# Kernel optimization log

Hardware: AMD Instinct MI355X
Metric: run time of the kernel (lower is better)

Reference implementation:

```python
import jax, jax.numpy as jnp
import numpy as np

N = 50000   # nodes
E = 800000  # edges (avg degree 16)
D = 128     # node_dim == hidden_dim
L = 5       # propagation_depth


def setup_inputs() -> dict:
    key = jax.random.key(0)
    k1, k2, k3, k4 = jax.random.split(key, 4)
    feat = jax.random.normal(k1, (N, D), dtype=jnp.float32)
    src = jax.random.randint(k2, (E,), 0, N)
    dst = jax.random.randint(k3, (E,), 0, N)
    # Glorot-ish init for the 5 stacked GraphConv weights
    W = jax.random.normal(k4, (L, D, D), dtype=jnp.float32) * (1.0 / np.sqrt(D))
    b = jnp.zeros((L, D), dtype=jnp.float32)
    return {"feat": feat, "src": src, "dst": dst, "W": W, "b": b}


def reference(feat, src, dst, W, b):
    # DGL GraphConv, norm='both':
    #   h' = relu( D_in^{-1/2} * (sum over in-edges of D_out^{-1/2} h_src) @ W + b )
    ones = jnp.ones((src.shape[0],), dtype=feat.dtype)
    deg_out = jnp.maximum(jax.ops.segment_sum(ones, src, num_segments=N), 1.0)
    deg_in = jnp.maximum(jax.ops.segment_sum(ones, dst, num_segments=N), 1.0)
    norm_src = deg_out ** -0.5  # [N]
    norm_dst = deg_in ** -0.5   # [N]

    h = feat
    for l in range(W.shape[0]):
        hs = h * norm_src[:, None]                                   # [N, D]
        agg = jax.ops.segment_sum(hs[src], dst, num_segments=N)      # sparse SpMM: [N, D]
        h = jax.nn.relu(agg * norm_dst[:, None] @ W[l] + b[l])       # [N, D]
    return h
```

## Files before the change

kernel.cpp:

```cpp
#include <hip/hip_runtime.h>

#define DD 128
#define NBC 64

__device__ __forceinline__ unsigned int rtn16(float f) {
  unsigned int u = __float_as_uint(f);
  return (u + 0x7FFFu + ((u >> 16) & 1u)) >> 16;
}
#define UNPK_LO(u) __uint_as_float((u) << 16)
#define UNPK_HI(u) __uint_as_float((u) & 0xFFFF0000u)


__global__ __launch_bounds__(256) void hist2_kernel(const int* __restrict__ src,
                                                    const int* __restrict__ dst,
                                                    unsigned int* __restrict__ hsrc,
                                                    unsigned int* __restrict__ hdst,
                                                    int e, int n, int ec) {
  __shared__ unsigned int h[32768];
  int c = blockIdx.x & (NBC - 1);
  bool is_src = blockIdx.x >= NBC;
  const int* __restrict__ ids = is_src ? src : dst;
  unsigned int* __restrict__ out = is_src ? hsrc : hdst;
  int nw = (n + 1) >> 1;
  for (int w = threadIdx.x; w < nw; w += 256) h[w] = 0u;
  __syncthreads();
  int lo = c * ec;
  int hi = lo + ec; if (hi > e) hi = e;
  for (int i = lo + threadIdx.x; i < hi; i += 256) {
    int d = ids[i];
    atomicAdd(&h[d >> 1], (d & 1) ? 0x10000u : 1u);
  }
  __syncthreads();
  for (int w = threadIdx.x; w < nw; w += 256) out[(size_t)c * nw + w] = h[w];
}

__global__ __launch_bounds__(256) void degnorm_prefix_kernel(
    const unsigned int* __restrict__ hsrc, unsigned int* __restrict__ hdst,
    int* __restrict__ deg_in, float* __restrict__ norm_src,
    float* __restrict__ norm_dst, int n) {
  int nw = (n + 1) >> 1;
  int w = blockIdx.x * 256 + threadIdx.x;
  if (w >= nw) return;
  unsigned int slo = 0, shi = 0, dlo = 0, dhi = 0;
  for (int c = 0; c < NBC; ++c) {
    unsigned int a = hsrc[(size_t)c * nw + w];
    slo += a & 0xFFFFu; shi += a >> 16;
    size_t idx = (size_t)c * nw + w;
    unsigned int v = hdst[idx];
    hdst[idx] = dlo | (dhi << 16);
    dlo += v & 0xFFFFu; dhi += v >> 16;
  }
  int n0 = 2 * w, n1 = 2 * w + 1;
  deg_in[n0] = (int)dlo;
  norm_src[n0] = 1.0f / sqrtf((float)(slo < 1u ? 1u : slo));
  norm_dst[n0] = 1.0f / sqrtf((float)(dlo < 1u ? 1u : dlo));
  if (n1 < n) {
    deg_in[n1] = (int)dhi;
    norm_src[n1] = 1.0f / sqrtf((float)(shi < 1u ? 1u : shi));
    norm_dst[n1] = 1.0f / sqrtf((float)(dhi < 1u ? 1u : dhi));
  }
}

__global__ __launch_bounds__(256) void scan_partial_kernel(const int* __restrict__ cnt,
                                                           int* __restrict__ bsum, int n) {
  __shared__ int ws[4];
  int tid = threadIdx.x;
  int base = blockIdx.x * 2048 + tid * 8;
  int s = 0;
#pragma unroll
  for (int i = 0; i < 8; ++i) {
    int id = base + i;
    if (id < n) s += cnt[id];
  }
#pragma unroll
  for (int d = 32; d; d >>= 1) s += __shfl_xor(s, d, 64);
  int lane = tid & 63, wid = tid >> 6;
  if (lane == 0) ws[wid] = s;
  __syncthreads();
  if (tid == 0) bsum[blockIdx.x] = ws[0] + ws[1] + ws[2] + ws[3];
}

__global__ __launch_bounds__(64) void scan_bsum_kernel(int* __restrict__ bsum, int nb) {
  int lane = threadIdx.x;
  int run = 0;
  for (int base = 0; base < nb; base += 64) {
    int id = base + lane;
    int v = (id < nb) ? bsum[id] : 0;
    int sc = v;
#pragma unroll
    for (int d = 1; d < 64; d <<= 1) {
      int t = __shfl_up(sc, d, 64);
      if (lane >= d) sc += t;
    }
    if (id < nb) bsum[id] = run + sc - v;
    run += __shfl(sc, 63, 64);
  }
}

__global__ __launch_bounds__(256) void scan_final_kernel(const int* __restrict__ cnt,
                                                         const int* __restrict__ bsum,
                                                         int* __restrict__ row_ptr,
                                                         int n, int e_total) {
  __shared__ int ws[4];
  int tid = threadIdx.x, lane = tid & 63, wid = tid >> 6;
  int base = blockIdx.x * 2048 + tid * 8;
  int v[8];
  int s = 0;
#pragma unroll
  for (int i = 0; i < 8; ++i) {
    int id = base + i;
    v[i] = (id < n) ? cnt[id] : 0;
    s += v[i];
  }
  int sc = s;
#pragma unroll
  for (int d = 1; d < 64; d <<= 1) {
    int t = __shfl_up(sc, d, 64);
    if (lane >= d) sc += t;
  }
  if (lane == 63) ws[wid] = sc;
  __syncthreads();
  int woff = 0;
  for (int w = 0; w < wid; ++w) woff += ws[w];
  int off = bsum[blockIdx.x] + woff + (sc - s);
#pragma unroll
  for (int i = 0; i < 8; ++i) {
    int id = base + i;
    if (id < n) {
      row_ptr[id] = off;
      off += v[i];
    }
  }
  if (blockIdx.x == 0 && tid == 0) row_ptr[n] = e_total;
}

__global__ __launch_bounds__(256) void fillx_kernel(const int* __restrict__ src,
                                                    const int* __restrict__ dst,
                                                    const unsigned int* __restrict__ hdst,
                                                    const int* __restrict__ row_ptr,
                                                    int* __restrict__ adj,
                                                    int e, int n, int ec) {
  __shared__ unsigned int h[32768];
  int c = blockIdx.x;
  int nw = (n + 1) >> 1;
  for (int w = threadIdx.x; w < nw; w += 256) h[w] = 0u;
  __syncthreads();
  int lo = c * ec;
  int hi = lo + ec; if (hi > e) hi = e;
  for (int i = lo + threadIdx.x; i < hi; i += 256) {
    int s = src[i];
    int d = dst[i];
    unsigned int old = atomicAdd(&h[d >> 1], (d & 1) ? 0x10000u : 1u);
    unsigned int rank = (d & 1) ? (old >> 16) : (old & 0xFFFFu);
    unsigned int pre = hdst[(size_t)c * nw + (d >> 1)];
    pre = (d & 1) ? (pre >> 16) : (pre & 0xFFFFu);
    adj[row_ptr[d] + (int)pre + (int)rank] = s;
  }
}

__global__ __launch_bounds__(256) void prescale_kernel(const float* __restrict__ feat,
                                                       const float* __restrict__ ns,
                                                       unsigned short* __restrict__ ga,
                                                       unsigned short* __restrict__ gb,
                                                       int n) {
  int i = blockIdx.x * 256 + threadIdx.x;
  if (i >= (n + 1) * 32) return;
  if (i >= n * 32) {
    ((uint2*)ga)[i] = make_uint2(0u, 0u);
    ((uint2*)gb)[i] = make_uint2(0u, 0u);
    return;
  }
  float4 v = ((const float4*)feat)[i];
  float s = ns[i >> 5];
  unsigned int p0 = rtn16(v.x * s), p1 = rtn16(v.y * s);
  unsigned int p2 = rtn16(v.z * s), p3 = rtn16(v.w * s);
  ((uint2*)ga)[i] = make_uint2(p0 | (p1 << 16), p2 | (p3 << 16));
}

__global__ __launch_bounds__(256) void layer_kernel(const unsigned short* __restrict__ gin,
                                                    unsigned short* __restrict__ goutb,
                                                    float* __restrict__ goutf,
                                                    const int* __restrict__ adj,
                                                    const int* __restrict__ row_ptr,
                                                    const float* __restrict__ ns,
                                                    const float* __restrict__ ndv,
                                                    const float* __restrict__ W,
                                                    const float* __restrict__ bias,
                                                    int n, int last) {
  __shared__ float Xs[32][DD];
  int tid = threadIdx.x;
  int lane = tid & 63;
  int wv = tid >> 6;
  int m4 = lane & 15;
  int q = lane >> 4;
  int row0 = blockIdx.x * 32;
  const uint4* g4 = (const uint4*)gin;

  for (int r = wv; r < 32; r += 4) {
    int node = row0 + r;
    float a0 = 0.f, a1 = 0.f, a2 = 0.f, a3 = 0.f;
    float a4 = 0.f, a5 = 0.f, a6 = 0.f, a7 = 0.f;
    float scale = 0.f;
#define ACC8(v)                                        \
  a0 += UNPK_LO(v.x); a1 += UNPK_HI(v.x);              \
  a2 += UNPK_LO(v.y); a3 += UNPK_HI(v.y);              \
  a4 += UNPK_LO(v.z); a5 += UNPK_HI(v.z);              \
  a6 += UNPK_LO(v.w); a7 += UNPK_HI(v.w);
    if (node < n) {
      scale = ndv[node];
      int beg = row_ptr[node];
      int end = row_ptr[node + 1];
      for (int j = beg; j < end; j += 16) {
        int i0 = j + q;
        int i1 = j + 4 + q;
        int i2 = j + 8 + q;
        int i3 = j + 12 + q;
        int e0 = (i0 < end) ? adj[i0] : n;
        int e1 = (i1 < end) ? adj[i1] : n;
        int e2 = (i2 < end) ? adj[i2] : n;
        int e3 = (i3 < end) ? adj[i3] : n;
        uint4 v0 = g4[(size_t)e0 * 16 + m4];
        uint4 v1 = g4[(size_t)e1 * 16 + m4];
        uint4 v2 = g4[(size_t)e2 * 16 + m4];
        uint4 v3 = g4[(size_t)e3 * 16 + m4];
        ACC8(v0); ACC8(v1); ACC8(v2); ACC8(v3);
      }
    }
#undef ACC8
    a0 += __shfl_xor(a0, 16, 64); a0 += __shfl_xor(a0, 32, 64);
    a1 += __shfl_xor(a1, 16, 64); a1 += __shfl_xor(a1, 32, 64);
    a2 += __shfl_xor(a2, 16, 64); a2 += __shfl_xor(a2, 32, 64);
    a3 += __shfl_xor(a3, 16, 64); a3 += __shfl_xor(a3, 32, 64);
    a4 += __shfl_xor(a4, 16, 64); a4 += __shfl_xor(a4, 32, 64);
    a5 += __shfl_xor(a5, 16, 64); a5 += __shfl_xor(a5, 32, 64);
    a6 += __shfl_xor(a6, 16, 64); a6 += __shfl_xor(a6, 32, 64);
    a7 += __shfl_xor(a7, 16, 64); a7 += __shfl_xor(a7, 32, 64);
    if (q == 0) {
      float* xp = &Xs[r][m4 * 8];
      xp[0] = a0 * scale; xp[1] = a1 * scale;
      xp[2] = a2 * scale; xp[3] = a3 * scale;
      xp[4] = a4 * scale; xp[5] = a5 * scale;
      xp[6] = a6 * scale; xp[7] = a7 * scale;
    }
  }
  __syncthreads();

  int tx = tid & 31;
  int ty = tid >> 5;
  float acc[4][4] = {};
  const float4* wp0 = (const float4*)W + tx;
  for (int k4 = 0; k4 < DD / 4; ++k4) {
    const float4* wp = wp0 + (size_t)k4 * 4 * 32;
    float4 w0 = wp[0];
    float4 w1 = wp[32];
    float4 w2 = wp[64];
    float4 w3 = wp[96];
#pragma unroll
    for (int i = 0; i < 4; ++i) {
      float4 x = *(const float4*)&Xs[ty * 4 + i][k4 * 4];
      acc[i][0] = fmaf(x.x, w0.x, acc[i][0]);
      acc[i][1] = fmaf(x.x, w0.y, acc[i][1]);
      acc[i][2] = fmaf(x.x, w0.z, acc[i][2]);
      acc[i][3] = fmaf(x.x, w0.w, acc[i][3]);
      acc[i][0] = fmaf(x.y, w1.x, acc[i][0]);
      acc[i][1] = fmaf(x.y, w1.y, acc[i][1]);
      acc[i][2] = fmaf(x.y, w1.z, acc[i][2]);
      acc[i][3] = fmaf(x.y, w1.w, acc[i][3]);
      acc[i][0] = fmaf(x.z, w2.x, acc[i][0]);
      acc[i][1] = fmaf(x.z, w2.y, acc[i][1]);
      acc[i][2] = fmaf(x.z, w2.z, acc[i][2]);
      acc[i][3] = fmaf(x.z, w2.w, acc[i][3]);
      acc[i][0] = fmaf(x.w, w3.x, acc[i][0]);
      acc[i][1] = fmaf(x.w, w3.y, acc[i][1]);
      acc[i][2] = fmaf(x.w, w3.z, acc[i][2]);
      acc[i][3] = fmaf(x.w, w3.w, acc[i][3]);
    }
  }
  float4 bv = *(const float4*)(bias + tx * 4);
#pragma unroll
  for (int i = 0; i < 4; ++i) {
    int r = row0 + ty * 4 + i;
    if (r < n) {
      float4 o;
      o.x = fmaxf(acc[i][0] + bv.x, 0.f);
      o.y = fmaxf(acc[i][1] + bv.y, 0.f);
      o.z = fmaxf(acc[i][2] + bv.z, 0.f);
      o.w = fmaxf(acc[i][3] + bv.w, 0.f);
      if (last) {
        *(float4*)(goutf + (size_t)r * DD + tx * 4) = o;
      } else {
        float s = ns[r];
        unsigned int p0 = rtn16(o.x * s), p1 = rtn16(o.y * s);
        unsigned int p2 = rtn16(o.z * s), p3 = rtn16(o.w * s);
        ((uint2*)(goutb + (size_t)r * DD))[tx] =
            make_uint2(p0 | (p1 << 16), p2 | (p3 << 16));
      }
    }
  }
}


extern "C" void kernel_launch(void* const* d_in, const int* in_sizes, int n_in,
                              void* d_out, int out_size, void* d_ws, size_t ws_size,
                              hipStream_t stream) {
  const float* feat = (const float*)d_in[0];
  const int* src = (const int*)d_in[1];
  const int* dst = (const int*)d_in[2];
  const float* W = (const float*)d_in[3];
  const float* b = (const float*)d_in[4];
  const int N = in_sizes[0] / DD;
  const int E = in_sizes[1];
  const int L = in_sizes[3] / (DD * DD);
  const int NW = (N + 1) >> 1;
  const int EC = (E + NBC - 1) / NBC;

  char* p = (char*)d_ws;
  auto alloc = [&](size_t bytes) {
    void* r = (void*)p;
    p += (bytes + 255) & ~(size_t)255;
    return r;
  };
  int* deg_in = (int*)alloc((size_t)N * 4);
  int* row_ptr = (int*)alloc(((size_t)N + 1) * 4);
  int* adj = (int*)alloc((size_t)E * 4);
  float* norm_src = (float*)alloc((size_t)N * 4);
  float* norm_dst = (float*)alloc((size_t)N * 4);
  int* bsum = (int*)alloc(((size_t)N / 2048 + 2) * 4);
  unsigned int* hsrc = (unsigned int*)alloc((size_t)NBC * NW * 4);
  unsigned int* hdst = (unsigned int*)alloc((size_t)NBC * NW * 4);
  unsigned short* ga = (unsigned short*)alloc(((size_t)N + 1) * DD * 2);
  unsigned short* gb = (unsigned short*)alloc(((size_t)N + 1) * DD * 2);

  const int nb = (N + 2047) / 2048;
  const int nwb = (NW + 255) / 256;

  hist2_kernel<<<2 * NBC, 256, 0, stream>>>(src, dst, hsrc, hdst, E, N, EC);
  degnorm_prefix_kernel<<<nwb, 256, 0, stream>>>(hsrc, hdst, deg_in, norm_src,
                                                 norm_dst, N);
  scan_partial_kernel<<<nb, 256, 0, stream>>>(deg_in, bsum, N);
  scan_bsum_kernel<<<1, 64, 0, stream>>>(bsum, nb);
  scan_final_kernel<<<nb, 256, 0, stream>>>(deg_in, bsum, row_ptr, N, E);
  fillx_kernel<<<NBC, 256, 0, stream>>>(src, dst, hdst, row_ptr, adj, E, N, EC);

  float* out_f = (float*)d_out;
  prescale_kernel<<<((N + 1) * 32 + 255) / 256, 256, 0, stream>>>(feat, norm_src,
                                                                  ga, gb, N);
  for (int l = 0; l < L; ++l) {
    const unsigned short* gi = (l & 1) ? gb : ga;
    unsigned short* go = (l & 1) ? ga : gb;
    int last = (l == L - 1) ? 1 : 0;
    layer_kernel<<<(N + 31) / 32, 256, 0, stream>>>(
        gi, go, out_f, adj, row_ptr, norm_src, norm_dst,
        W + (size_t)l * DD * DD, b + (size_t)l * DD, N, last);
  }
}
```

Baseline: 435.2 us.

## Fuse scan partials into degree kernel and batch two-row neighbor gathers

The per-block degree sums for the row-pointer scan are now computed inside the degree/normalization kernel, which removes the separate scan_partial pass. The scan blocks shrink to 512 nodes so they line up with that kernel's blocks. The layer kernel's gather loop now handles two rows per wave at once and issues the first 32 neighbor index loads and feature loads for each row up front, to raise memory-level parallelism. It also sets a 4-blocks-per-SM launch bound. This costs higher register pressure and may cause spilling.

```diff
diff --git a/kernel.cpp b/kernel.cpp
--- a/kernel.cpp
+++ b/kernel.cpp
@@ -37,44 +37,36 @@
 __global__ __launch_bounds__(256) void degnorm_prefix_kernel(
     const unsigned int* __restrict__ hsrc, unsigned int* __restrict__ hdst,
     int* __restrict__ deg_in, float* __restrict__ norm_src,
-    float* __restrict__ norm_dst, int n) {
+    float* __restrict__ norm_dst, int* __restrict__ bsum, int n) {
+  __shared__ int ws[4];
   int nw = (n + 1) >> 1;
-  int w = blockIdx.x * 256 + threadIdx.x;
-  if (w >= nw) return;
+  int tid = threadIdx.x, lane = tid & 63, wid = tid >> 6;
+  int w = blockIdx.x * 256 + tid;
   unsigned int slo = 0, shi = 0, dlo = 0, dhi = 0;
-  for (int c = 0; c < NBC; ++c) {
-    unsigned int a = hsrc[(size_t)c * nw + w];
-    slo += a & 0xFFFFu; shi += a >> 16;
-    size_t idx = (size_t)c * nw + w;
-    unsigned int v = hdst[idx];
-    hdst[idx] = dlo | (dhi << 16);
-    dlo += v & 0xFFFFu; dhi += v >> 16;
-  }
-  int n0 = 2 * w, n1 = 2 * w + 1;
-  deg_in[n0] = (int)dlo;
-  norm_src[n0] = 1.0f / sqrtf((float)(slo < 1u ? 1u : slo));
-  norm_dst[n0] = 1.0f / sqrtf((float)(dlo < 1u ? 1u : dlo));
-  if (n1 < n) {
-    deg_in[n1] = (int)dhi;
-    norm_src[n1] = 1.0f / sqrtf((float)(shi < 1u ? 1u : shi));
-    norm_dst[n1] = 1.0f / sqrtf((float)(dhi < 1u ? 1u : dhi));
-  }
-}
-
-__global__ __launch_bounds__(256) void scan_partial_kernel(const int* __restrict__ cnt,
-                                                           int* __restrict__ bsum, int n) {
-  __shared__ int ws[4];
-  int tid = threadIdx.x;
-  int base = blockIdx.x * 2048 + tid * 8;
-  int s = 0;
-#pragma unroll
-  for (int i = 0; i < 8; ++i) {
-    int id = base + i;
-    if (id < n) s += cnt[id];
-  }
+  if (w < nw) {
+    for (int c = 0; c < NBC; ++c) {
+      unsigned int a = hsrc[(size_t)c * nw + w];
+      slo += a & 0xFFFFu; shi += a >> 16;
+      size_t idx = (size_t)c * nw + w;
+      unsigned int v = hdst[idx];
+      hdst[idx] = dlo | (dhi << 16);
+      dlo += v & 0xFFFFu; dhi += v >> 16;
+    }
+    int n0 = 2 * w, n1 = 2 * w + 1;
+    deg_in[n0] = (int)dlo;
+    norm_src[n0] = 1.0f / sqrtf((float)(slo < 1u ? 1u : slo));
+    norm_dst[n0] = 1.0f / sqrtf((float)(dlo < 1u ? 1u : dlo));
+    if (n1 < n) {
+      deg_in[n1] = (int)dhi;
+      norm_src[n1] = 1.0f / sqrtf((float)(shi < 1u ? 1u : shi));
+      norm_dst[n1] = 1.0f / sqrtf((float)(dhi < 1u ? 1u : dhi));
+    } else {
+      dhi = 0;
+    }
+  }
+  int s = (int)(dlo + dhi);
 #pragma unroll
   for (int d = 32; d; d >>= 1) s += __shfl_xor(s, d, 64);
-  int lane = tid & 63, wid = tid >> 6;
   if (lane == 0) ws[wid] = s;
   __syncthreads();
   if (tid == 0) bsum[blockIdx.x] = ws[0] + ws[1] + ws[2] + ws[3];
@@ -103,15 +95,10 @@
                                                          int n, int e_total) {
   __shared__ int ws[4];
   int tid = threadIdx.x, lane = tid & 63, wid = tid >> 6;
-  int base = blockIdx.x * 2048 + tid * 8;
-  int v[8];
-  int s = 0;
-#pragma unroll
-  for (int i = 0; i < 8; ++i) {
-    int id = base + i;
-    v[i] = (id < n) ? cnt[id] : 0;
-    s += v[i];
-  }
+  int id0 = blockIdx.x * 512 + tid * 2;
+  int v0 = (id0 < n) ? cnt[id0] : 0;
+  int v1 = (id0 + 1 < n) ? cnt[id0 + 1] : 0;
+  int s = v0 + v1;
   int sc = s;
 #pragma unroll
   for (int d = 1; d < 64; d <<= 1) {
@@ -121,16 +108,10 @@
   if (lane == 63) ws[wid] = sc;
   __syncthreads();
   int woff = 0;
-  for (int w = 0; w < wid; ++w) woff += ws[w];
+  for (int w2 = 0; w2 < wid; ++w2) woff += ws[w2];
   int off = bsum[blockIdx.x] + woff + (sc - s);
-#pragma unroll
-  for (int i = 0; i < 8; ++i) {
-    int id = base + i;
-    if (id < n) {
-      row_ptr[id] = off;
-      off += v[i];
-    }
-  }
+  if (id0 < n) row_ptr[id0] = off;
+  if (id0 + 1 < n) row_ptr[id0 + 1] = off + v0;
   if (blockIdx.x == 0 && tid == 0) row_ptr[n] = e_total;
 }
 
@@ -177,16 +158,12 @@
   ((uint2*)ga)[i] = make_uint2(p0 | (p1 << 16), p2 | (p3 << 16));
 }
 
-__global__ __launch_bounds__(256) void layer_kernel(const unsigned short* __restrict__ gin,
-                                                    unsigned short* __restrict__ goutb,
-                                                    float* __restrict__ goutf,
-                                                    const int* __restrict__ adj,
-                                                    const int* __restrict__ row_ptr,
-                                                    const float* __restrict__ ns,
-                                                    const float* __restrict__ ndv,
-                                                    const float* __restrict__ W,
-                                                    const float* __restrict__ bias,
-                                                    int n, int last) {
+__global__ __launch_bounds__(256, 4) void layer_kernel(
+    const unsigned short* __restrict__ gin, unsigned short* __restrict__ goutb,
+    float* __restrict__ goutf, const int* __restrict__ adj,
+    const int* __restrict__ row_ptr, const float* __restrict__ ns,
+    const float* __restrict__ ndv, const float* __restrict__ W,
+    const float* __restrict__ bias, int n, int last) {
   __shared__ float Xs[32][DD];
   int tid = threadIdx.x;
   int lane = tid & 63;
@@ -196,53 +173,86 @@
   int row0 = blockIdx.x * 32;
   const uint4* g4 = (const uint4*)gin;
 
-  for (int r = wv; r < 32; r += 4) {
-    int node = row0 + r;
-    float a0 = 0.f, a1 = 0.f, a2 = 0.f, a3 = 0.f;
-    float a4 = 0.f, a5 = 0.f, a6 = 0.f, a7 = 0.f;
-    float scale = 0.f;
-#define ACC8(v)                                        \
-  a0 += UNPK_LO(v.x); a1 += UNPK_HI(v.x);              \
-  a2 += UNPK_LO(v.y); a3 += UNPK_HI(v.y);              \
-  a4 += UNPK_LO(v.z); a5 += UNPK_HI(v.z);              \
-  a6 += UNPK_LO(v.w); a7 += UNPK_HI(v.w);
-    if (node < n) {
-      scale = ndv[node];
-      int beg = row_ptr[node];
-      int end = row_ptr[node + 1];
-      for (int j = beg; j < end; j += 16) {
-        int i0 = j + q;
-        int i1 = j + 4 + q;
-        int i2 = j + 8 + q;
-        int i3 = j + 12 + q;
-        int e0 = (i0 < end) ? adj[i0] : n;
-        int e1 = (i1 < end) ? adj[i1] : n;
-        int e2 = (i2 < end) ? adj[i2] : n;
-        int e3 = (i3 < end) ? adj[i3] : n;
-        uint4 v0 = g4[(size_t)e0 * 16 + m4];
-        uint4 v1 = g4[(size_t)e1 * 16 + m4];
-        uint4 v2 = g4[(size_t)e2 * 16 + m4];
-        uint4 v3 = g4[(size_t)e3 * 16 + m4];
-        ACC8(v0); ACC8(v1); ACC8(v2); ACC8(v3);
-      }
-    }
+#define ACC8(a, v)                                   \
+  a[0] += UNPK_LO(v.x); a[1] += UNPK_HI(v.x);        \
+  a[2] += UNPK_LO(v.y); a[3] += UNPK_HI(v.y);        \
+  a[4] += UNPK_LO(v.z); a[5] += UNPK_HI(v.z);        \
+  a[6] += UNPK_LO(v.w); a[7] += UNPK_HI(v.w);
+
+  for (int p = 0; p < 4; ++p) {
+    int rA = wv + p * 8;
+    int rB = rA + 4;
+    int nodeA = row0 + rA, nodeB = row0 + rB;
+    int begA = 0, endA = 0, begB = 0, endB = 0;
+    float scA = 0.f, scB = 0.f;
+    if (nodeA < n) { begA = row_ptr[nodeA]; endA = row_ptr[nodeA + 1]; scA = ndv[nodeA]; }
+    if (nodeB < n) { begB = row_ptr[nodeB]; endB = row_ptr[nodeB + 1]; scB = ndv[nodeB]; }
+    int eA[8], eB[8];
+#pragma unroll
+    for (int k = 0; k < 8; ++k) {
+      int iA = begA + 4 * k + q;
+      eA[k] = (iA < endA) ? adj[iA] : n;
+    }
+#pragma unroll
+    for (int k = 0; k < 8; ++k) {
+      int iB = begB + 4 * k + q;
+      eB[k] = (iB < endB) ? adj[iB] : n;
+    }
+    uint4 vA[8], vB[8];
+#pragma unroll
+    for (int k = 0; k < 8; ++k) vA[k] = g4[(size_t)eA[k] * 16 + m4];
+#pragma unroll
+    for (int k = 0; k < 8; ++k) vB[k] = g4[(size_t)eB[k] * 16 + m4];
+    float aA[8] = {}, aB[8] = {};
+#pragma unroll
+    for (int k = 0; k < 8; ++k) { ACC8(aA, vA[k]); }
+#pragma unroll
+    for (int k = 0; k < 8; ++k) { ACC8(aB, vB[k]); }
+    for (int j = begA + 32; j < endA; j += 16) {
+      int i0 = j + q, i1 = j + 4 + q, i2 = j + 8 + q, i3 = j + 12 + q;
+      int e0 = (i0 < endA) ? adj[i0] : n;
+      int e1 = (i1 < endA) ? adj[i1] : n;
+      int e2 = (i2 < endA) ? adj[i2] : n;
+      int e3 = (i3 < endA) ? adj[i3] : n;
+      uint4 t0 = g4[(size_t)e0 * 16 + m4];
+      uint4 t1 = g4[(size_t)e1 * 16 + m4];
+      uint4 t2 = g4[(size_t)e2 * 16 + m4];
+      uint4 t3 = g4[(size_t)e3 * 16 + m4];
+      ACC8(aA, t0); ACC8(aA, t1); ACC8(aA, t2); ACC8(aA, t3);
+    }
+    for (int j = begB + 32; j < endB; j += 16) {
+      int i0 = j + q, i1 = j + 4 + q, i2 = j + 8 + q, i3 = j + 12 + q;
+      int e0 = (i0 < endB) ? adj[i0] : n;
+      int e1 = (i1 < endB) ? adj[i1] : n;
+      int e2 = (i2 < endB) ? adj[i2] : n;
+      int e3 = (i3 < endB) ? adj[i3] : n;
+      uint4 t0 = g4[(size_t)e0 * 16 + m4];
+      uint4 t1 = g4[(size_t)e1 * 16 + m4];
+      uint4 t2 = g4[(size_t)e2 * 16 + m4];
+      uint4 t3 = g4[(size_t)e3 * 16 + m4];
+      ACC8(aB, t0); ACC8(aB, t1); ACC8(aB, t2); ACC8(aB, t3);
+    }
+#pragma unroll
+    for (int k = 0; k < 8; ++k) {
+      aA[k] += __shfl_xor(aA[k], 16, 64);
+      aA[k] += __shfl_xor(aA[k], 32, 64);
+      aB[k] += __shfl_xor(aB[k], 16, 64);
+      aB[k] += __shfl_xor(aB[k], 32, 64);
+    }
+    if (q == 0) {
+      float* xp = &Xs[rA][m4 * 8];
+      xp[0] = aA[0] * scA; xp[1] = aA[1] * scA;
+      xp[2] = aA[2] * scA; xp[3] = aA[3] * scA;
+      xp[4] = aA[4] * scA; xp[5] = aA[5] * scA;
+      xp[6] = aA[6] * scA; xp[7] = aA[7] * scA;
+      float* yp = &Xs[rB][m4 * 8];
+      yp[0] = aB[0] * scB; yp[1] = aB[1] * scB;
+      yp[2] = aB[2] * scB; yp[3] = aB[3] * scB;
+      yp[4] = aB[4] * scB; yp[5] = aB[5] * scB;
+      yp[6] = aB[6] * scB; yp[7] = aB[7] * scB;
+    }
+  }
 #undef ACC8
-    a0 += __shfl_xor(a0, 16, 64); a0 += __shfl_xor(a0, 32, 64);
-    a1 += __shfl_xor(a1, 16, 64); a1 += __shfl_xor(a1, 32, 64);
-    a2 += __shfl_xor(a2, 16, 64); a2 += __shfl_xor(a2, 32, 64);
-    a3 += __shfl_xor(a3, 16, 64); a3 += __shfl_xor(a3, 32, 64);
-    a4 += __shfl_xor(a4, 16, 64); a4 += __shfl_xor(a4, 32, 64);
-    a5 += __shfl_xor(a5, 16, 64); a5 += __shfl_xor(a5, 32, 64);
-    a6 += __shfl_xor(a6, 16, 64); a6 += __shfl_xor(a6, 32, 64);
-    a7 += __shfl_xor(a7, 16, 64); a7 += __shfl_xor(a7, 32, 64);
-    if (q == 0) {
-      float* xp = &Xs[r][m4 * 8];
-      xp[0] = a0 * scale; xp[1] = a1 * scale;
-      xp[2] = a2 * scale; xp[3] = a3 * scale;
-      xp[4] = a4 * scale; xp[5] = a5 * scale;
-      xp[6] = a6 * scale; xp[7] = a7 * scale;
-    }
-  }
   __syncthreads();
 
   int tx = tid & 31;
@@ -325,21 +335,19 @@
   int* adj = (int*)alloc((size_t)E * 4);
   float* norm_src = (float*)alloc((size_t)N * 4);
   float* norm_dst = (float*)alloc((size_t)N * 4);
-  int* bsum = (int*)alloc(((size_t)N / 2048 + 2) * 4);
+  int* bsum = (int*)alloc(((size_t)N / 512 + 2) * 4);
   unsigned int* hsrc = (unsigned int*)alloc((size_t)NBC * NW * 4);
   unsigned int* hdst = (unsigned int*)alloc((size_t)NBC * NW * 4);
   unsigned short* ga = (unsigned short*)alloc(((size_t)N + 1) * DD * 2);
   unsigned short* gb = (unsigned short*)alloc(((size_t)N + 1) * DD * 2);
 
-  const int nb = (N + 2047) / 2048;
   const int nwb = (NW + 255) / 256;
 
   hist2_kernel<<<2 * NBC, 256, 0, stream>>>(src, dst, hsrc, hdst, E, N, EC);
   degnorm_prefix_kernel<<<nwb, 256, 0, stream>>>(hsrc, hdst, deg_in, norm_src,
-                                                 norm_dst, N);
-  scan_partial_kernel<<<nb, 256, 0, stream>>>(deg_in, bsum, N);
-  scan_bsum_kernel<<<1, 64, 0, stream>>>(bsum, nb);
-  scan_final_kernel<<<nb, 256, 0, stream>>>(deg_in, bsum, row_ptr, N, E);
+                                                 norm_dst, bsum, N);
+  scan_bsum_kernel<<<1, 64, 0, stream>>>(bsum, nwb);
+  scan_final_kernel<<<nwb, 256, 0, stream>>>(deg_in, bsum, row_ptr, N, E);
   fillx_kernel<<<NBC, 256, 0, stream>>>(src, dst, hdst, row_ptr, adj, E, N, EC);
 
   float* out_f = (float*)d_out;
```

Result: no change. 434.3 us (-0.2%).
